# Kernel optimization log

Measured on AMD Instinct MI355X. Metric: run time of the kernel, lower is better.

## Reference

```python
import jax, jax.numpy as jnp
import numpy as np
import math

B_SZ, T, D_IN, D_OUT, N = 8, 4096, 128, 128, 256
MAX_PHASE, RMIN, RMAX = math.pi, 0.0, 1.0


def setup_inputs() -> dict:
    key = jax.random.key(0)
    ks = jax.random.split(key, 9)
    x = jax.random.normal(ks[0], (B_SZ, T, D_IN), dtype=jnp.float32)
    # lambda parameterization exactly as in LRU.__init__
    u1 = jax.random.uniform(ks[1], (N,), minval=1e-4, maxval=1.0)
    u2 = jax.random.uniform(ks[2], (N,), minval=1e-4, maxval=1.0)
    nu_log = jnp.log(-0.5 * jnp.log(u1 * (RMAX + RMIN) * (RMAX - RMIN) + RMIN ** 2))
    theta_log = jnp.log(MAX_PHASE * u2)
    lam_abs = jnp.exp(-jnp.exp(nu_log))
    gamma_log = jnp.log(jnp.sqrt(1.0 - jnp.square(lam_abs)))
    B_re = jax.random.normal(ks[3], (N, D_IN)) / math.sqrt(2 * D_IN)
    B_im = jax.random.normal(ks[4], (N, D_IN)) / math.sqrt(2 * D_IN)
    C_re = jax.random.normal(ks[5], (D_OUT, N)) / math.sqrt(N)
    C_im = jax.random.normal(ks[6], (D_OUT, N)) / math.sqrt(N)
    D = jax.random.normal(ks[7], (D_OUT, D_IN)) / math.sqrt(D_IN)
    return {"x": x, "nu_log": nu_log, "theta_log": theta_log, "gamma_log": gamma_log,
            "B_re": B_re, "B_im": B_im, "C_re": C_re, "C_im": C_im, "D": D}


def _binary_op_diag(e1, e2):
    a1, b1 = e1
    a2, b2 = e2
    return a1 * a2, a2 * b1 + b2


def reference(x, nu_log, theta_log, gamma_log, B_re, B_im, C_re, C_im, D):
    # ss_params()
    lam_abs = jnp.exp(-jnp.exp(nu_log))
    phase = jnp.exp(theta_log)
    lam = (lam_abs * jnp.cos(phase) + 1j * (lam_abs * jnp.sin(phase))).astype(jnp.complex64)  # [N]
    gammas = jnp.exp(gamma_log)[:, None]
    Bc = (gammas * (B_re + 1j * B_im)).astype(jnp.complex64)  # [N, D_IN]
    Cc = (C_re + 1j * C_im).astype(jnp.complex64)             # [D_OUT, N]
    # diagonal complex linear recurrence via associative scan over time
    Bu = x.astype(Bc.dtype) @ Bc.T                            # [B, T, N] complex
    lam_el = jnp.broadcast_to(lam, Bu.shape)                  # [B, T, N]
    _, states = jax.lax.associative_scan(_binary_op_diag, (lam_el, Bu), axis=1)
    y = jnp.real(states @ Cc.T) + x @ D.T                     # [B, T, D_OUT]
    return y
```

## Files before the change

kernel.cpp:

```cpp
#include <hip/hip_runtime.h>
#include <math.h>

#define B_SZ 8
#define T_LEN 4096
#define D_IN 128
#define D_OUT 128
#define N_ST 256
#define BT (B_SZ * T_LEN)
#define CHUNK 64
#define NCHUNK (T_LEN / CHUNK)
#define NBLK (B_SZ * NCHUNK)

typedef __attribute__((ext_vector_type(8))) short short8;
typedef __attribute__((ext_vector_type(4))) float f32x4;
typedef unsigned int uint;
typedef unsigned short ushort;

static __device__ __forceinline__ short f2bf(float f) {
  union { float f; uint u; } v; v.f = f;
  uint r = v.u + 0x7FFFu + ((v.u >> 16) & 1u);
  return (short)(r >> 16);
}
static __device__ __forceinline__ float bf2f(uint h) {
  union { uint u; float f; } v; v.u = h << 16;
  return v.f;
}
static __device__ __forceinline__ uint pack2(float a, float b) {
  return (uint)(ushort)f2bf(a) | ((uint)(ushort)f2bf(b) << 16);
}

__global__ __launch_bounds__(256) void k0_setup(
    const float* __restrict__ x,
    const float* __restrict__ nu_log, const float* __restrict__ theta_log,
    const float* __restrict__ gamma_log,
    const float* __restrict__ B_re, const float* __restrict__ B_im,
    const float* __restrict__ C_re, const float* __restrict__ C_im,
    const float* __restrict__ Dm,
    short* __restrict__ Wf1, short* __restrict__ Wf2,
    float2* __restrict__ lampow2, short* __restrict__ xbf) {
  int blk = blockIdx.x;
  if (blk < 320) {
    int idx = blk * 256 + threadIdx.x;
    if (idx < 16 * 512 * 8) {
      int j = idx & 7, col = (idx >> 3) & 511, kg = idx >> 12;
      int k = kg * 8 + j;
      int n = col >> 1, ri = col & 1;
      float g = expf(gamma_log[n]);
      float v = g * (ri ? B_im[n * D_IN + k] : B_re[n * D_IN + k]);
      Wf1[idx] = f2bf(v);
    }
    if (idx < 80 * 128 * 8) {
      int j = idx & 7, d = (idx >> 3) & 127, kg = idx >> 10;
      int k = kg * 8 + j;
      float v;
      if (k < 512) {
        int n = k >> 1;
        v = (k & 1) ? -C_im[d * N_ST + n] : C_re[d * N_ST + n];
      } else {
        v = Dm[d * D_IN + (k - 512)];
      }
      Wf2[idx] = f2bf(v);
    }
  } else if (blk < 385) {
    int j = blk - 320;
    int n = threadIdx.x;
    float e_nu = expf(nu_log[n]);
    float phase = expf(theta_log[n]);
    float r = expf(-(float)j * e_nu);
    float a = (float)j * phase;
    float2 v; v.x = r * cosf(a); v.y = r * sinf(a);
    lampow2[j * N_ST + n] = v;
  } else {
    size_t i = (size_t)(blk - 385) * 256 + threadIdx.x;
    const float4* x4 = (const float4*)x;
    float4 a = x4[2 * i], b = x4[2 * i + 1];
    uint4 u;
    u.x = pack2(a.x, a.y); u.y = pack2(a.z, a.w);
    u.z = pack2(b.x, b.y); u.w = pack2(b.z, b.w);
    ((uint4*)xbf)[i] = u;
  }
}

__global__ __launch_bounds__(256, 2) void kA(
    const short* __restrict__ xbf, const short* __restrict__ Wf1,
    const float2* __restrict__ lampow2, float2* __restrict__ E) {
  __shared__ short bu[64 * 520];

  int bc = blockIdx.x;
  size_t row0 = (size_t)bc * CHUNK;
  int tid = threadIdx.x;
  int lane = tid & 63, w = tid >> 6;
  int m = lane & 15, q = lane >> 4;

  f32x4 acc[32];
#pragma unroll
  for (int ct = 0; ct < 32; ++ct) acc[ct] = (f32x4){0.f, 0.f, 0.f, 0.f};

  const short* xrow = xbf + (row0 + 16 * w + m) * D_IN;

  for (int ks = 0; ks < 4; ++ks) {
    short8 af = *(const short8*)(xrow + 32 * ks + 8 * q);
    const short* wbase = Wf1 + ((size_t)(4 * ks + q) * 512 + m) * 8;
#pragma unroll
    for (int ct = 0; ct < 32; ++ct) {
      short8 bf = *(const short8*)(wbase + 16 * ct * 8);
      acc[ct] = __builtin_amdgcn_mfma_f32_16x16x32_bf16(af, bf, acc[ct], 0, 0, 0);
    }
  }

#pragma unroll
  for (int ct = 0; ct < 32; ++ct) {
#pragma unroll
    for (int r = 0; r < 4; ++r) {
      bu[(16 * w + 4 * q + r) * 520 + 16 * ct + m] = f2bf(acc[ct][r]);
    }
  }
  __syncthreads();

  int n = tid;
  float2 lam = lampow2[N_ST + n];
  float sre = 0.f, sim = 0.f;
  for (int j = 0; j < CHUNK; ++j) {
    uint p = ((const uint*)(bu + j * 520))[n];
    float br = bf2f(p & 0xffffu), bi = bf2f(p >> 16);
    float nr = fmaf(lam.x, sre, fmaf(-lam.y, sim, br));
    float ni = fmaf(lam.x, sim, fmaf(lam.y, sre, bi));
    sre = nr; sim = ni;
  }
  float2 e; e.x = sre; e.y = sim;
  E[bc * N_ST + n] = e;
}

__global__ __launch_bounds__(256) void kB(
    const float2* __restrict__ E, const float2* __restrict__ lampow2,
    float2* __restrict__ P) {
  __shared__ float2 Es[NCHUNK * N_ST];

  int b = blockIdx.x;
  int tid = threadIdx.x;

  const float4* src = (const float4*)(E + (size_t)b * NCHUNK * N_ST);
  float4* dst = (float4*)Es;
#pragma unroll
  for (int it = 0; it < (NCHUNK * N_ST / 2) / 256; ++it) {
    dst[it * 256 + tid] = src[it * 256 + tid];
  }
  __syncthreads();

  int n = tid;
  float2 lamL = lampow2[CHUNK * N_ST + n];
  float cre = 0.f, cim = 0.f;
  for (int c = 0; c < NCHUNK; ++c) {
    size_t i = ((size_t)b * NCHUNK + c) * N_ST + n;
    float2 pv; pv.x = cre; pv.y = cim;
    P[i] = pv;
    float2 e = Es[c * N_ST + n];
    float nre = fmaf(lamL.x, cre, fmaf(-lamL.y, cim, e.x));
    float nim = fmaf(lamL.x, cim, fmaf(lamL.y, cre, e.y));
    cre = nre; cim = nim;
  }
}

__global__ __launch_bounds__(256, 2) void kC(
    const short* __restrict__ xbf, const short* __restrict__ Wf1,
    const float2* __restrict__ P, const float2* __restrict__ lampow2,
    const short* __restrict__ Wf2, float* __restrict__ y) {
  __shared__ short bu[64 * 520];

  int bc = blockIdx.x;
  size_t row0 = (size_t)bc * CHUNK;
  int tid = threadIdx.x;
  int lane = tid & 63, w = tid >> 6;
  int m = lane & 15, q = lane >> 4;

  f32x4 acc[32];
#pragma unroll
  for (int ct = 0; ct < 32; ++ct) acc[ct] = (f32x4){0.f, 0.f, 0.f, 0.f};

  const short* xrow = xbf + (row0 + 16 * w + m) * D_IN;

  for (int ks = 0; ks < 4; ++ks) {
    short8 af = *(const short8*)(xrow + 32 * ks + 8 * q);
    const short* wbase = Wf1 + ((size_t)(4 * ks + q) * 512 + m) * 8;
#pragma unroll
    for (int ct = 0; ct < 32; ++ct) {
      short8 bf = *(const short8*)(wbase + 16 * ct * 8);
      acc[ct] = __builtin_amdgcn_mfma_f32_16x16x32_bf16(af, bf, acc[ct], 0, 0, 0);
    }
  }

#pragma unroll
  for (int ct = 0; ct < 32; ++ct) {
#pragma unroll
    for (int r = 0; r < 4; ++r) {
      bu[(16 * w + 4 * q + r) * 520 + 16 * ct + m] = f2bf(acc[ct][r]);
    }
  }
  __syncthreads();

  {
    int n = tid;
    float2 lam = lampow2[N_ST + n];
    float sre = 0.f, sim = 0.f;
    for (int j = 0; j < CHUNK; ++j) {
      uint p = ((const uint*)(bu + j * 520))[n];
      float br = bf2f(p & 0xffffu), bi = bf2f(p >> 16);
      float nr = fmaf(lam.x, sre, fmaf(-lam.y, sim, br));
      float ni = fmaf(lam.x, sim, fmaf(lam.y, sre, bi));
      sre = nr; sim = ni;
      ((uint*)(bu + j * 520))[n] = pack2(sre, sim);
    }
  }
  __syncthreads();

  {
    int n4 = tid & 63, rblk = tid >> 6;
    float4 pA = *(const float4*)(P + (size_t)bc * N_ST + 4 * n4);
    float4 pB = *(const float4*)(P + (size_t)bc * N_ST + 4 * n4 + 2);
#pragma unroll
    for (int rr = 0; rr < 16; ++rr) {
      int row = rblk * 16 + rr;
      uint4 sp = *(const uint4*)(bu + row * 520 + 8 * n4);
      float4 lpa = *(const float4*)(lampow2 + ((size_t)(row + 1) * N_ST + 4 * n4));
      float4 lpb = *(const float4*)(lampow2 + ((size_t)(row + 1) * N_ST + 4 * n4 + 2));
      uint4 outv;
      {
        float sr = bf2f(sp.x & 0xffffu) + lpa.x * pA.x - lpa.y * pA.y;
        float si = bf2f(sp.x >> 16)     + lpa.x * pA.y + lpa.y * pA.x;
        outv.x = pack2(sr, si);
      }
      {
        float sr = bf2f(sp.y & 0xffffu) + lpa.z * pA.z - lpa.w * pA.w;
        float si = bf2f(sp.y >> 16)     + lpa.z * pA.w + lpa.w * pA.z;
        outv.y = pack2(sr, si);
      }
      {
        float sr = bf2f(sp.z & 0xffffu) + lpb.x * pB.x - lpb.y * pB.y;
        float si = bf2f(sp.z >> 16)     + lpb.x * pB.y + lpb.y * pB.x;
        outv.z = pack2(sr, si);
      }
      {
        float sr = bf2f(sp.w & 0xffffu) + lpb.z * pB.z - lpb.w * pB.w;
        float si = bf2f(sp.w >> 16)     + lpb.z * pB.w + lpb.w * pB.z;
        outv.w = pack2(sr, si);
      }
      *(uint4*)(bu + row * 520 + 8 * n4) = outv;
    }
  }
  __syncthreads();

  int rw = w & 1, ch = w >> 1;
  int arow0 = 32 * rw + m;

  short8 xa0[4], xa1[4];
#pragma unroll
  for (int t = 0; t < 4; ++t) {
    int g = 64 + 4 * t + q;
    xa0[t] = *(const short8*)(xbf + (row0 + arow0) * D_IN + (g - 64) * 8);
    xa1[t] = *(const short8*)(xbf + (row0 + arow0 + 16) * D_IN + (g - 64) * 8);
  }

  f32x4 acc2[2][4];
#pragma unroll
  for (int rt = 0; rt < 2; ++rt)
#pragma unroll
    for (int ci = 0; ci < 4; ++ci) acc2[rt][ci] = (f32x4){0.f, 0.f, 0.f, 0.f};

  for (int ks = 0; ks < 16; ++ks) {
    int g = 4 * ks + q;
    short8 af0 = *(const short8*)(bu + arow0 * 520 + 8 * g);
    short8 af1 = *(const short8*)(bu + (arow0 + 16) * 520 + 8 * g);
    const short* wbase = Wf2 + ((size_t)g * 128 + m) * 8;
#pragma unroll
    for (int ci = 0; ci < 4; ++ci) {
      int ctg = 4 * ch + ci;
      short8 bf = *(const short8*)(wbase + 16 * ctg * 8);
      acc2[0][ci] = __builtin_amdgcn_mfma_f32_16x16x32_bf16(af0, bf, acc2[0][ci], 0, 0, 0);
      acc2[1][ci] = __builtin_amdgcn_mfma_f32_16x16x32_bf16(af1, bf, acc2[1][ci], 0, 0, 0);
    }
  }
#pragma unroll
  for (int t = 0; t < 4; ++t) {
    int g = 64 + 4 * t + q;
    const short* wbase = Wf2 + ((size_t)g * 128 + m) * 8;
#pragma unroll
    for (int ci = 0; ci < 4; ++ci) {
      int ctg = 4 * ch + ci;
      short8 bf = *(const short8*)(wbase + 16 * ctg * 8);
      acc2[0][ci] = __builtin_amdgcn_mfma_f32_16x16x32_bf16(xa0[t], bf, acc2[0][ci], 0, 0, 0);
      acc2[1][ci] = __builtin_amdgcn_mfma_f32_16x16x32_bf16(xa1[t], bf, acc2[1][ci], 0, 0, 0);
    }
  }

#pragma unroll
  for (int ci = 0; ci < 4; ++ci) {
    int ctg = 4 * ch + ci;
#pragma unroll
    for (int rt = 0; rt < 2; ++rt) {
#pragma unroll
      for (int r = 0; r < 4; ++r) {
        y[(row0 + 32 * rw + 16 * rt + 4 * q + r) * D_OUT + 16 * ctg + m] = acc2[rt][ci][r];
      }
    }
  }
}

extern "C" void kernel_launch(void* const* d_in, const int* in_sizes, int n_in,
                              void* d_out, int out_size, void* d_ws, size_t ws_size,
                              hipStream_t stream) {
  const float* x         = (const float*)d_in[0];
  const float* nu_log    = (const float*)d_in[1];
  const float* theta_log = (const float*)d_in[2];
  const float* gamma_log = (const float*)d_in[3];
  const float* B_re      = (const float*)d_in[4];
  const float* B_im      = (const float*)d_in[5];
  const float* C_re      = (const float*)d_in[6];
  const float* C_im      = (const float*)d_in[7];
  const float* Dm        = (const float*)d_in[8];
  float* y = (float*)d_out;

  char* wp = (char*)d_ws;
  float2* lampow2 = (float2*)wp; wp += (size_t)(CHUNK + 1) * N_ST * sizeof(float2);
  short*  Wf1     = (short*)wp;  wp += (size_t)16 * 512 * 8 * sizeof(short);
  short*  Wf2     = (short*)wp;  wp += (size_t)80 * 128 * 8 * sizeof(short);
  float2* E       = (float2*)wp; wp += (size_t)NBLK * N_ST * sizeof(float2);
  float2* P       = (float2*)wp; wp += (size_t)NBLK * N_ST * sizeof(float2);
  short*  xbf     = (short*)wp;  wp += (size_t)BT * D_IN * sizeof(short);

  hipLaunchKernelGGL(k0_setup, dim3(385 + BT * D_IN / 8 / 256), dim3(256), 0, stream,
                     x, nu_log, theta_log, gamma_log, B_re, B_im, C_re, C_im,
                     Dm, Wf1, Wf2, lampow2, xbf);
  hipLaunchKernelGGL(kA, dim3(NBLK), dim3(256), 0, stream,
                     xbf, Wf1, lampow2, E);
  hipLaunchKernelGGL(kB, dim3(B_SZ), dim3(256), 0, stream,
                     E, lampow2, P);
  hipLaunchKernelGGL(kC, dim3(NBLK), dim3(256), 0, stream,
                     xbf, Wf1, P, lampow2, Wf2, y);
}
```

Measured before the change: 140.2 us.

## Fuse scan kernels into one persistent kernel with grid barriers

Merges the chunk-local scan, the cross-chunk carry scan and the output kernel into a single launch that uses atomic-counter grid barriers. Chunk states stay in LDS, so the first Bu GEMM and the chunk scan run once per chunk instead of twice. The bf16 copy of x is dropped and x is converted to bf16 on the fly from fp32. The carry-scan loop also prefetches E eight chunks ahead. This removes launch gaps and redundant recomputation, but relies on all 512 blocks being co-resident for the barrier to avoid deadlock, and reads twice as many bytes of x per load.

```diff
diff --git a/kernel.cpp b/kernel.cpp
--- a/kernel.cpp
+++ b/kernel.cpp
@@ -28,16 +28,23 @@
 static __device__ __forceinline__ uint pack2(float a, float b) {
   return (uint)(ushort)f2bf(a) | ((uint)(ushort)f2bf(b) << 16);
 }
-
-__global__ __launch_bounds__(256) void k0_setup(
-    const float* __restrict__ x,
+static __device__ __forceinline__ short8 cvt8(const float* __restrict__ p) {
+  float4 a = *(const float4*)p;
+  float4 b = *(const float4*)(p + 4);
+  union { short8 s; uint4 u; } r;
+  r.u.x = pack2(a.x, a.y); r.u.y = pack2(a.z, a.w);
+  r.u.z = pack2(b.x, b.y); r.u.w = pack2(b.z, b.w);
+  return r.s;
+}
+
+__global__ __launch_bounds__(256) void k0w(
     const float* __restrict__ nu_log, const float* __restrict__ theta_log,
     const float* __restrict__ gamma_log,
     const float* __restrict__ B_re, const float* __restrict__ B_im,
     const float* __restrict__ C_re, const float* __restrict__ C_im,
     const float* __restrict__ Dm,
     short* __restrict__ Wf1, short* __restrict__ Wf2,
-    float2* __restrict__ lampow2, short* __restrict__ xbf) {
+    float2* __restrict__ lampow2, uint* __restrict__ bar) {
   int blk = blockIdx.x;
   if (blk < 320) {
     int idx = blk * 256 + threadIdx.x;
@@ -61,8 +68,9 @@
       }
       Wf2[idx] = f2bf(v);
     }
-  } else if (blk < 385) {
+  } else {
     int j = blk - 320;
+    if (j == 64 && threadIdx.x == 0) *bar = 0;
     int n = threadIdx.x;
     float e_nu = expf(nu_log[n]);
     float phase = expf(theta_log[n]);
@@ -70,20 +78,25 @@
     float a = (float)j * phase;
     float2 v; v.x = r * cosf(a); v.y = r * sinf(a);
     lampow2[j * N_ST + n] = v;
-  } else {
-    size_t i = (size_t)(blk - 385) * 256 + threadIdx.x;
-    const float4* x4 = (const float4*)x;
-    float4 a = x4[2 * i], b = x4[2 * i + 1];
-    uint4 u;
-    u.x = pack2(a.x, a.y); u.y = pack2(a.z, a.w);
-    u.z = pack2(b.x, b.y); u.w = pack2(b.z, b.w);
-    ((uint4*)xbf)[i] = u;
-  }
-}
-
-__global__ __launch_bounds__(256, 2) void kA(
-    const short* __restrict__ xbf, const short* __restrict__ Wf1,
-    const float2* __restrict__ lampow2, float2* __restrict__ E) {
+  }
+}
+
+static __device__ __forceinline__ void gridbar(uint* bar, uint target) {
+  __syncthreads();
+  if (threadIdx.x == 0) {
+    __threadfence();
+    atomicAdd(bar, 1u);
+    while (atomicAdd(bar, 0u) < target) __builtin_amdgcn_s_sleep(2);
+    __threadfence();
+  }
+  __syncthreads();
+}
+
+__global__ __launch_bounds__(256, 2) void kF(
+    const float* __restrict__ x, const short* __restrict__ Wf1,
+    const float2* __restrict__ lampow2, const short* __restrict__ Wf2,
+    float2* __restrict__ E, float2* __restrict__ P, float* __restrict__ y,
+    uint* __restrict__ bar) {
   __shared__ short bu[64 * 520];
 
   int bc = blockIdx.x;
@@ -96,91 +109,10 @@
 #pragma unroll
   for (int ct = 0; ct < 32; ++ct) acc[ct] = (f32x4){0.f, 0.f, 0.f, 0.f};
 
-  const short* xrow = xbf + (row0 + 16 * w + m) * D_IN;
+  const float* xrowf = x + (row0 + 16 * w + m) * D_IN;
 
   for (int ks = 0; ks < 4; ++ks) {
-    short8 af = *(const short8*)(xrow + 32 * ks + 8 * q);
-    const short* wbase = Wf1 + ((size_t)(4 * ks + q) * 512 + m) * 8;
-#pragma unroll
-    for (int ct = 0; ct < 32; ++ct) {
-      short8 bf = *(const short8*)(wbase + 16 * ct * 8);
-      acc[ct] = __builtin_amdgcn_mfma_f32_16x16x32_bf16(af, bf, acc[ct], 0, 0, 0);
-    }
-  }
-
-#pragma unroll
-  for (int ct = 0; ct < 32; ++ct) {
-#pragma unroll
-    for (int r = 0; r < 4; ++r) {
-      bu[(16 * w + 4 * q + r) * 520 + 16 * ct + m] = f2bf(acc[ct][r]);
-    }
-  }
-  __syncthreads();
-
-  int n = tid;
-  float2 lam = lampow2[N_ST + n];
-  float sre = 0.f, sim = 0.f;
-  for (int j = 0; j < CHUNK; ++j) {
-    uint p = ((const uint*)(bu + j * 520))[n];
-    float br = bf2f(p & 0xffffu), bi = bf2f(p >> 16);
-    float nr = fmaf(lam.x, sre, fmaf(-lam.y, sim, br));
-    float ni = fmaf(lam.x, sim, fmaf(lam.y, sre, bi));
-    sre = nr; sim = ni;
-  }
-  float2 e; e.x = sre; e.y = sim;
-  E[bc * N_ST + n] = e;
-}
-
-__global__ __launch_bounds__(256) void kB(
-    const float2* __restrict__ E, const float2* __restrict__ lampow2,
-    float2* __restrict__ P) {
-  __shared__ float2 Es[NCHUNK * N_ST];
-
-  int b = blockIdx.x;
-  int tid = threadIdx.x;
-
-  const float4* src = (const float4*)(E + (size_t)b * NCHUNK * N_ST);
-  float4* dst = (float4*)Es;
-#pragma unroll
-  for (int it = 0; it < (NCHUNK * N_ST / 2) / 256; ++it) {
-    dst[it * 256 + tid] = src[it * 256 + tid];
-  }
-  __syncthreads();
-
-  int n = tid;
-  float2 lamL = lampow2[CHUNK * N_ST + n];
-  float cre = 0.f, cim = 0.f;
-  for (int c = 0; c < NCHUNK; ++c) {
-    size_t i = ((size_t)b * NCHUNK + c) * N_ST + n;
-    float2 pv; pv.x = cre; pv.y = cim;
-    P[i] = pv;
-    float2 e = Es[c * N_ST + n];
-    float nre = fmaf(lamL.x, cre, fmaf(-lamL.y, cim, e.x));
-    float nim = fmaf(lamL.x, cim, fmaf(lamL.y, cre, e.y));
-    cre = nre; cim = nim;
-  }
-}
-
-__global__ __launch_bounds__(256, 2) void kC(
-    const short* __restrict__ xbf, const short* __restrict__ Wf1,
-    const float2* __restrict__ P, const float2* __restrict__ lampow2,
-    const short* __restrict__ Wf2, float* __restrict__ y) {
-  __shared__ short bu[64 * 520];
-
-  int bc = blockIdx.x;
-  size_t row0 = (size_t)bc * CHUNK;
-  int tid = threadIdx.x;
-  int lane = tid & 63, w = tid >> 6;
-  int m = lane & 15, q = lane >> 4;
-
-  f32x4 acc[32];
-#pragma unroll
-  for (int ct = 0; ct < 32; ++ct) acc[ct] = (f32x4){0.f, 0.f, 0.f, 0.f};
-
-  const short* xrow = xbf + (row0 + 16 * w + m) * D_IN;
-
-  for (int ks = 0; ks < 4; ++ks) {
-    short8 af = *(const short8*)(xrow + 32 * ks + 8 * q);
+    short8 af = cvt8(xrowf + 32 * ks + 8 * q);
     const short* wbase = Wf1 + ((size_t)(4 * ks + q) * 512 + m) * 8;
 #pragma unroll
     for (int ct = 0; ct < 32; ++ct) {
@@ -210,8 +142,42 @@
       sre = nr; sim = ni;
       ((uint*)(bu + j * 520))[n] = pack2(sre, sim);
     }
-  }
-  __syncthreads();
+    float2 e; e.x = sre; e.y = sim;
+    E[bc * N_ST + n] = e;
+  }
+  gridbar(bar, NBLK);
+
+  if (bc < B_SZ) {
+    int b = bc, n = tid;
+    float2 lamL = lampow2[CHUNK * N_ST + n];
+    float2 eb0, eb1, eb2, eb3, eb4, eb5, eb6, eb7;
+    const float2* Eb = E + (size_t)b * NCHUNK * N_ST;
+    eb0 = Eb[0 * N_ST + n]; eb1 = Eb[1 * N_ST + n];
+    eb2 = Eb[2 * N_ST + n]; eb3 = Eb[3 * N_ST + n];
+    eb4 = Eb[4 * N_ST + n]; eb5 = Eb[5 * N_ST + n];
+    eb6 = Eb[6 * N_ST + n]; eb7 = Eb[7 * N_ST + n];
+    float cre = 0.f, cim = 0.f;
+#pragma unroll
+    for (int c = 0; c < NCHUNK; ++c) {
+      float2 pv; pv.x = cre; pv.y = cim;
+      P[((size_t)b * NCHUNK + c) * N_ST + n] = pv;
+      float2 e;
+      switch (c & 7) {
+        case 0: e = eb0; if (c + 8 < NCHUNK) eb0 = Eb[(c + 8) * N_ST + n]; break;
+        case 1: e = eb1; if (c + 8 < NCHUNK) eb1 = Eb[(c + 8) * N_ST + n]; break;
+        case 2: e = eb2; if (c + 8 < NCHUNK) eb2 = Eb[(c + 8) * N_ST + n]; break;
+        case 3: e = eb3; if (c + 8 < NCHUNK) eb3 = Eb[(c + 8) * N_ST + n]; break;
+        case 4: e = eb4; if (c + 8 < NCHUNK) eb4 = Eb[(c + 8) * N_ST + n]; break;
+        case 5: e = eb5; if (c + 8 < NCHUNK) eb5 = Eb[(c + 8) * N_ST + n]; break;
+        case 6: e = eb6; if (c + 8 < NCHUNK) eb6 = Eb[(c + 8) * N_ST + n]; break;
+        default: e = eb7; if (c + 8 < NCHUNK) eb7 = Eb[(c + 8) * N_ST + n]; break;
+      }
+      float nre = fmaf(lamL.x, cre, fmaf(-lamL.y, cim, e.x));
+      float nim = fmaf(lamL.x, cim, fmaf(lamL.y, cre, e.y));
+      cre = nre; cim = nim;
+    }
+  }
+  gridbar(bar, 2 * NBLK);
 
   {
     int n4 = tid & 63, rblk = tid >> 6;
@@ -255,9 +221,8 @@
   short8 xa0[4], xa1[4];
 #pragma unroll
   for (int t = 0; t < 4; ++t) {
-    int g = 64 + 4 * t + q;
-    xa0[t] = *(const short8*)(xbf + (row0 + arow0) * D_IN + (g - 64) * 8);
-    xa1[t] = *(const short8*)(xbf + (row0 + arow0 + 16) * D_IN + (g - 64) * 8);
+    xa0[t] = cvt8(x + (row0 + arow0) * D_IN + 32 * t + 8 * q);
+    xa1[t] = cvt8(x + (row0 + arow0 + 16) * D_IN + 32 * t + 8 * q);
   }
 
   f32x4 acc2[2][4];
@@ -325,15 +290,11 @@
   short*  Wf2     = (short*)wp;  wp += (size_t)80 * 128 * 8 * sizeof(short);
   float2* E       = (float2*)wp; wp += (size_t)NBLK * N_ST * sizeof(float2);
   float2* P       = (float2*)wp; wp += (size_t)NBLK * N_ST * sizeof(float2);
-  short*  xbf     = (short*)wp;  wp += (size_t)BT * D_IN * sizeof(short);
-
-  hipLaunchKernelGGL(k0_setup, dim3(385 + BT * D_IN / 8 / 256), dim3(256), 0, stream,
-                     x, nu_log, theta_log, gamma_log, B_re, B_im, C_re, C_im,
-                     Dm, Wf1, Wf2, lampow2, xbf);
-  hipLaunchKernelGGL(kA, dim3(NBLK), dim3(256), 0, stream,
-                     xbf, Wf1, lampow2, E);
-  hipLaunchKernelGGL(kB, dim3(B_SZ), dim3(256), 0, stream,
-                     E, lampow2, P);
-  hipLaunchKernelGGL(kC, dim3(NBLK), dim3(256), 0, stream,
-                     xbf, Wf1, P, lampow2, Wf2, y);
-}
+  uint*   bar     = (uint*)wp;   wp += 256;
+
+  hipLaunchKernelGGL(k0w, dim3(385), dim3(256), 0, stream,
+                     nu_log, theta_log, gamma_log, B_re, B_im, C_re, C_im,
+                     Dm, Wf1, Wf2, lampow2, bar);
+  hipLaunchKernelGGL(kF, dim3(NBLK), dim3(256), 0, stream,
+                     x, Wf1, lampow2, Wf2, E, P, y, bar);
+}
```

After: 190.3 us. 1.36x slower.
